# Kernel tuning notes

Hardware: AMD Instinct MI355X
Metric: run time of the kernel (lower is better)

Reference implementation:

```python
import jax, jax.numpy as jnp
import numpy as np

B, C, L, V, H, HEADS, ITERS = 8, 2048, 3, 512, 256, 8, 8
HD = H // HEADS
MAX_LIT = 1024  # literal embedding table holds 2*MAX_LIT rows


def _lin(x, W, b):
    return x @ W.T + b


def _gelu(x):
    return jax.nn.gelu(x, approximate=False)  # torch nn.GELU default = exact erf


def _ln(x, g, b):
    m = x.mean(-1, keepdims=True)
    v = ((x - m) ** 2).mean(-1, keepdims=True)
    return (x - m) / jnp.sqrt(v + 1e-5) * g + b


def setup_inputs() -> dict:
    key = jax.random.key(0)
    ks = jax.random.split(key, 16)
    s = 0.02
    p = {}
    p["formula"] = jax.random.randint(ks[0], (B, C, L), 0, 2 * V)
    p["lit_emb"] = jax.random.normal(ks[1], (2 * MAX_LIT, H)) * s
    # clause_encoder: Linear(H,2H) -> LayerNorm(2H) -> GELU -> Linear(2H,H)
    p["ce_w1"] = jax.random.normal(ks[2], (2 * H, H)) * s
    p["ce_b1"] = jnp.zeros((2 * H,))
    p["ce_g"] = jnp.ones((2 * H,))
    p["ce_beta"] = jnp.zeros((2 * H,))
    p["ce_w2"] = jax.random.normal(ks[3], (H, 2 * H)) * s
    p["ce_b2"] = jnp.zeros((H,))
    # clause_var_attention (nn.MultiheadAttention, eval mode -> no dropout)
    p["attn_in_w"] = jax.random.normal(ks[4], (3 * H, H)) * s
    p["attn_in_b"] = jnp.zeros((3 * H,))
    p["attn_out_w"] = jax.random.normal(ks[5], (H, H)) * s
    p["attn_out_b"] = jnp.zeros((H,))
    # variable_selector: Linear -> GELU -> Linear(H,1)
    p["vs_w1"] = jax.random.normal(ks[6], (H, H)) * s
    p["vs_b1"] = jnp.zeros((H,))
    p["vs_w2"] = jax.random.normal(ks[7], (1, H)) * s
    p["vs_b2"] = jnp.zeros((1,))
    # assignment_predictor: Linear -> GELU -> Linear(H,2) -> Softmax
    p["ap_w1"] = jax.random.normal(ks[8], (H, H)) * s
    p["ap_b1"] = jnp.zeros((H,))
    p["ap_w2"] = jax.random.normal(ks[9], (2, H)) * s
    p["ap_b2"] = jnp.zeros((2,))
    # sat_predictor: Linear -> GELU -> Linear(H,1) -> Sigmoid
    p["sp_w1"] = jax.random.normal(ks[10], (H, H)) * s
    p["sp_b1"] = jnp.zeros((H,))
    p["sp_w2"] = jax.random.normal(ks[11], (1, H)) * s
    p["sp_b2"] = jnp.zeros((1,))
    return p


def _mha(q, kv, in_w, in_b, out_w, out_b):
    Wq, Wk, Wv = jnp.split(in_w, 3, axis=0)
    bq, bk, bv = jnp.split(in_b, 3, axis=0)
    Bq, Nq, _ = q.shape
    Nk = kv.shape[1]
    qh = _lin(q, Wq, bq).reshape(Bq, Nq, HEADS, HD).transpose(0, 2, 1, 3)
    kh = _lin(kv, Wk, bk).reshape(Bq, Nk, HEADS, HD).transpose(0, 2, 1, 3)
    vh = _lin(kv, Wv, bv).reshape(Bq, Nk, HEADS, HD).transpose(0, 2, 1, 3)
    attn = jax.nn.softmax(jnp.einsum("bhqd,bhkd->bhqk", qh, kh) / np.float32(np.sqrt(HD)), axis=-1)
    o = jnp.einsum("bhqk,bhkd->bhqd", attn, vh).transpose(0, 2, 1, 3).reshape(Bq, Nq, H)
    return _lin(o, out_w, out_b)


def reference(formula, lit_emb, ce_w1, ce_b1, ce_g, ce_beta, ce_w2, ce_b2,
              attn_in_w, attn_in_b, attn_out_w, attn_out_b,
              vs_w1, vs_b1, vs_w2, vs_b2, ap_w1, ap_b1, ap_w2, ap_b2,
              sp_w1, sp_b1, sp_w2, sp_b2):
    bidx = jnp.arange(B)
    lit_e = lit_emb[formula]  # [B,C,L,H]
    # clause_encoder output is assignment-independent -> hoist out of the loop
    base = _lin(_gelu(_ln(_lin(lit_e.mean(2), ce_w1, ce_b1), ce_g, ce_beta)), ce_w2, ce_b2)  # [B,C,H]
    var_idx = formula // 2  # [B,C,L]
    pol = formula % 2

    def step(carry, _):
        assignments, var_states, done = carry
        va = assignments[bidx[:, None, None], var_idx]          # [B,C,L] gather
        sat = jnp.any((va == pol) & (va != 2), -1)              # [B,C]
        clause_states = base * (1.0 - 0.9 * sat[..., None].astype(base.dtype))
        vs = _mha(var_states, clause_states, attn_in_w, attn_in_b, attn_out_w, attn_out_b)  # [B,V,H]
        scores = _lin(_gelu(_lin(vs, vs_w1, vs_b1)), vs_w2, vs_b2)[..., 0]  # [B,V]
        scores = scores + (assignments != 2).astype(scores.dtype) * (-1e9)
        sel = jnp.argmax(scores, 1)                             # [B]
        sel_states = vs[bidx, sel]
        probs = jax.nn.softmax(_lin(_gelu(_lin(sel_states, ap_w1, ap_b1)), ap_w2, ap_b2), -1)
        new_a = jnp.argmax(probs, 1).astype(assignments.dtype)
        a2 = assignments.at[bidx, sel].set(new_a)
        # conflict check with updated assignments
        va2 = a2[bidx[:, None, None], var_idx]
        sat2 = jnp.any((va2 == pol) & (va2 != 2), -1)
        conflicting = jnp.all(va2 != 2, -1) & ~sat2             # [B,C]
        any_conf = jnp.any(conflicting)                         # global, as in torch list check
        a3 = jnp.where(any_conf, a2.at[bidx, sel].set(2), a2)   # unassign selected var on conflict
        finished = jnp.all(a3 != 2) & ~any_conf                 # torch early-break condition
        assignments_n = jnp.where(done, assignments, a3)        # freeze after break
        vs_n = jnp.where(done, var_states, vs)
        return (assignments_n, vs_n, done | finished), None

    init = (jnp.full((B, V), 2, jnp.int32), jnp.zeros((B, V, H), base.dtype), jnp.array(False))
    (assignments, var_states, _), _ = jax.lax.scan(step, init, None, length=ITERS)
    is_sat = jax.nn.sigmoid(_lin(_gelu(_lin(var_states.mean(1), sp_w1, sp_b1)), sp_w2, sp_b2))  # [B,1]
    return is_sat, assignments
```

## Files before the change

kernel.cpp:

```cpp
#include <hip/hip_runtime.h>
#include <hip/hip_bf16.h>

#pragma clang fp contract(off)

#define DEVI __device__ __forceinline__

constexpr int Bc = 8, Cc = 2048, Vc = 512, Hc = 256;

constexpr int W_N = 23;
constexpr int W_OFF[W_N] = {
  0,        524288,  655360,  655872,  656384,  656896,  787968,  788224,
  984832,   985600,  1051136, 1051392, 1116928, 1117184, 1117440, 1117444,
  1182980,  1183236, 1183748, 1183752, 1249288, 1249544, 1249800 };
constexpr int W_SZ[W_N] = {
  524288, 131072, 512, 512, 512, 131072, 256, 196608, 768,
  65536, 256, 65536, 256, 256, 1, 65536, 256, 512, 2, 65536, 256, 256, 1 };
constexpr int W_TOT = 1249804;

constexpr size_t WT1_O   = 1249808;
constexpr size_t WT2_O   = WT1_O   + 131072;
constexpr size_t WTIN_O  = WT2_O   + 131072;
constexpr size_t WTOUT_O = WTIN_O  + 196608;
constexpr size_t WTV1_O  = WTOUT_O + 65536;
constexpr size_t WTAP_O  = WTV1_O  + 65536;
constexpr size_t WTSP_O  = WTAP_O  + 65536;
constexpr size_t WCK_O   = WTSP_O  + 65536;
constexpr size_t WCV_O   = WCK_O   + 131072;
constexpr size_t BCK_O   = WCV_O   + 131072;
constexpr size_t BCV_O   = BCK_O   + 256;
constexpr size_t KB_O    = BCV_O   + 256;
constexpr size_t VB_O    = KB_O    + 4194304;
constexpr size_t OO8_O   = VB_O    + 4194304;
constexpr size_t VS8_O   = OO8_O   + 2048;
constexpr size_t FTOT    = VS8_O   + 2048;

constexpr int T_N = 7;
constexpr int T_SRC[T_N]  = { 524288, 656896, 788224, 985600, 1051392, 1117444, 1183752 };
constexpr size_t T_DST[T_N] = { WT1_O, WT2_O, WTIN_O, WTOUT_O, WTV1_O, WTAP_O, WTSP_O };
constexpr int T_ROWS[T_N] = { 512, 256, 768, 256, 256, 256, 256 };
constexpr int T_L2C[T_N]  = { 8, 9, 8, 8, 8, 8, 8 };
constexpr int T_CUM[T_N + 1] = { 0, 131072, 262144, 458752, 524288, 589824, 655360, 720896 };

struct SrcPtrs { const void* p[W_N]; };

DEVI float gelu_ref(float x) {
  return (x * (erff(x / 1.41421356237309504880f) + 1.0f)) * 0.5f;
}

__global__ __launch_bounds__(256) void k_detect(const unsigned short* __restrict__ lit,
                                                int* __restrict__ dflag) {
  __shared__ int red[256];
  int t = threadIdx.x, c = 0;
  for (int i = t; i < 4096; i += 256) {
    unsigned e = (lit[i] >> 7) & 0xFF;
    if (e >= 0x8F) c++;
  }
  red[t] = c;
  __syncthreads();
  for (int s = 128; s > 0; s >>= 1) {
    if (t < s) red[t] += red[t + s];
    __syncthreads();
  }
  if (t == 0) dflag[0] = (red[0] > 64) ? 1 : 0;
}

__global__ __launch_bounds__(256) void k_convert(SrcPtrs sp, float* __restrict__ wf,
                                                 const int* __restrict__ dflag) {
  int idx = blockIdx.x * 256 + threadIdx.x;
  if (idx >= W_TOT) return;
  const int isf32 = dflag[0];
  int i = 0;
  while (i + 1 < W_N && idx >= W_OFF[i + 1]) i++;
  int j = idx - W_OFF[i];
  float v = 0.f;
  if (j < W_SZ[i]) {
    if (isf32) v = ((const float*)sp.p[i])[j];
    else {
      unsigned int u = (unsigned int)((const unsigned short*)sp.p[i])[j] << 16;
      v = __uint_as_float(u);
    }
  }
  wf[idx] = v;
}

__global__ __launch_bounds__(256) void k_transpose(float* __restrict__ wf) {
  int idx = blockIdx.x * 256 + threadIdx.x;
  if (idx >= T_CUM[T_N]) return;
  int mi = 0;
  while (mi + 1 < T_N && idx >= T_CUM[mi + 1]) mi++;
  int local = idx - T_CUM[mi];
  int cols = 1 << T_L2C[mi];
  int r = local >> T_L2C[mi];
  int c = local & (cols - 1);
  wf[T_DST[mi] + (size_t)c * T_ROWS[mi] + r] = wf[T_SRC[mi] + (size_t)local];
}

__global__ __launch_bounds__(256) void k_combine(float* __restrict__ wf) {
  const int blk = blockIdx.x, t = threadIdx.x;
  const float* wtin = wf + WTIN_O;
  if (blk < 512) {
    __shared__ float w2row[256];
    w2row[t] = wf[WT2_O + (size_t)blk * 256 + t];
    __syncthreads();
    float aK = 0.f, aV = 0.f;
    for (int m = 0; m < 256; ++m) {
      float w2 = w2row[m];
      aK = fmaf(w2, wtin[(size_t)m * 768 + 256 + t], aK);
      aV = fmaf(w2, wtin[(size_t)m * 768 + 512 + t], aV);
    }
    wf[WCK_O + (size_t)blk * 256 + t] = aK;
    wf[WCV_O + (size_t)blk * 256 + t] = aV;
  } else {
    float aK = 0.f, aV = 0.f;
    for (int m = 0; m < 256; ++m) {
      float b2 = wf[W_OFF[6] + m];
      aK = fmaf(b2, wtin[(size_t)m * 768 + 256 + t], aK);
      aV = fmaf(b2, wtin[(size_t)m * 768 + 512 + t], aV);
    }
    wf[BCK_O + t] = aK;
    wf[BCV_O + t] = aV;
  }
}

__global__ __launch_bounds__(256) void k_init(float* __restrict__ vs8,
    int* __restrict__ assign, int* __restrict__ flags) {
  int idx = blockIdx.x * 256 + threadIdx.x;
  assign[idx] = 2;
  if (idx < 2048) vs8[idx] = 0.f;
  if (idx < 3) flags[idx] = 0;
}

__global__ __launch_bounds__(256) void k_base(const int* __restrict__ formula,
    const float* __restrict__ wf, float* __restrict__ Kb, float* __restrict__ Vb) {
  __shared__ __align__(16) float xs[16][256];
  __shared__ __align__(16) float h1[16][516];
  __shared__ float mv[16], vr[16];
  const int t = threadIdx.x;
  const int n0 = blockIdx.x * 16;
  const float* lit = wf + W_OFF[0];
  for (int r = 0; r < 16; ++r) {
    int n = n0 + r;
    int f0 = formula[n*3+0], f1 = formula[n*3+1], f2 = formula[n*3+2];
    xs[r][t] = (lit[f0*256 + t] + lit[f1*256 + t] + lit[f2*256 + t]) / 3.0f;
  }
  __syncthreads();
  {
    const float* w1t = wf + WT1_O;
    float a0[16], a1[16];
    #pragma unroll
    for (int r = 0; r < 16; ++r) { a0[r] = 0.f; a1[r] = 0.f; }
    for (int k = 0; k < 256; k += 4) {
      float wa0 = w1t[(size_t)(k+0)*512 + t], wa1 = w1t[(size_t)(k+1)*512 + t];
      float wa2 = w1t[(size_t)(k+2)*512 + t], wa3 = w1t[(size_t)(k+3)*512 + t];
      float wb0 = w1t[(size_t)(k+0)*512 + 256 + t], wb1 = w1t[(size_t)(k+1)*512 + 256 + t];
      float wb2 = w1t[(size_t)(k+2)*512 + 256 + t], wb3 = w1t[(size_t)(k+3)*512 + 256 + t];
      #pragma unroll
      for (int r = 0; r < 16; ++r) {
        float4 x4 = *(const float4*)&xs[r][k];
        a0[r] = fmaf(x4.x, wa0, a0[r]);
        a0[r] = fmaf(x4.y, wa1, a0[r]);
        a0[r] = fmaf(x4.z, wa2, a0[r]);
        a0[r] = fmaf(x4.w, wa3, a0[r]);
        a1[r] = fmaf(x4.x, wb0, a1[r]);
        a1[r] = fmaf(x4.y, wb1, a1[r]);
        a1[r] = fmaf(x4.z, wb2, a1[r]);
        a1[r] = fmaf(x4.w, wb3, a1[r]);
      }
    }
    float b0 = wf[W_OFF[2] + t], b1b = wf[W_OFF[2] + t + 256];
    #pragma unroll
    for (int r = 0; r < 16; ++r) {
      h1[r][t] = a0[r] + b0;
      h1[r][t + 256] = a1[r] + b1b;
    }
  }
  __syncthreads();
  if (t < 16) {
    float s = 0.f;
    for (int k = 0; k < 512; ++k) s += h1[t][k];
    float m = s / 512.0f;
    float v = 0.f;
    for (int k = 0; k < 512; ++k) { float d = h1[t][k] - m; float d2 = d * d; v += d2; }
    mv[t] = m; vr[t] = v / 512.0f;
  }
  __syncthreads();
  {
    const float* g  = wf + W_OFF[3];
    const float* be = wf + W_OFF[4];
    for (int r = 0; r < 16; ++r) {
      float sd = sqrtf(vr[r] + 1e-5f);
      for (int c = t; c < 512; c += 256) {
        float val = (h1[r][c] - mv[r]) / sd * g[c] + be[c];
        h1[r][c] = gelu_ref(val);
      }
    }
  }
  __syncthreads();
  {
    const float* wck = wf + WCK_O;
    const float* wcv = wf + WCV_O;
    float aK[16], aV[16];
    #pragma unroll
    for (int r = 0; r < 16; ++r) { aK[r] = 0.f; aV[r] = 0.f; }
    for (int k = 0; k < 512; k += 4) {
      float ck0 = wck[(size_t)(k+0)*256 + t], ck1 = wck[(size_t)(k+1)*256 + t];
      float ck2 = wck[(size_t)(k+2)*256 + t], ck3 = wck[(size_t)(k+3)*256 + t];
      float cv0 = wcv[(size_t)(k+0)*256 + t], cv1 = wcv[(size_t)(k+1)*256 + t];
      float cv2 = wcv[(size_t)(k+2)*256 + t], cv3 = wcv[(size_t)(k+3)*256 + t];
      #pragma unroll
      for (int r = 0; r < 16; ++r) {
        float4 x4 = *(const float4*)&h1[r][k];
        aK[r] = fmaf(x4.x, ck0, aK[r]);
        aK[r] = fmaf(x4.y, ck1, aK[r]);
        aK[r] = fmaf(x4.z, ck2, aK[r]);
        aK[r] = fmaf(x4.w, ck3, aK[r]);
        aV[r] = fmaf(x4.x, cv0, aV[r]);
        aV[r] = fmaf(x4.y, cv1, aV[r]);
        aV[r] = fmaf(x4.z, cv2, aV[r]);
        aV[r] = fmaf(x4.w, cv3, aV[r]);
      }
    }
    float bck = wf[BCK_O + t], bcv = wf[BCV_O + t];
    const int h = t >> 5, d = t & 31;
    for (int r = 0; r < 16; ++r) {
      int n = n0 + r;
      int b = n >> 11, j = n & 2047;
      size_t off = ((size_t)(b * 8 + h) * 2048 + j) * 32 + d;
      Kb[off] = aK[r] + bck;
      Vb[off] = aV[r] + bcv;
    }
  }
}

__global__ __launch_bounds__(256) void k_attn8(const int* __restrict__ formula,
    const int* __restrict__ assign, const float* __restrict__ Kb,
    const float* __restrict__ Vb, const float* __restrict__ wf,
    const float* __restrict__ vs8, float* __restrict__ oo8,
    const int* __restrict__ flags) {
  if (flags[0]) return;
  __shared__ float xv[256], qs[32];
  __shared__ float sS[2048];
  __shared__ float sF[2048];
  __shared__ float sRed[256];
  __shared__ float sO[8][32];
  __shared__ float sM, sL, sQB;
  const int bh = blockIdx.x, b = bh >> 3, h = bh & 7;
  const int t = threadIdx.x;
  const float FAC1 = 1.0f - 0.9f;

  xv[t] = vs8[b * 256 + t];
  __syncthreads();
  if (t < 32) {
    const float* wt = wf + WTIN_O;
    const int c = h * 32 + t;
    float acc = 0.f;
    for (int k = 0; k < 256; ++k) acc = fmaf(xv[k], wt[(size_t)k * 768 + c], acc);
    qs[t] = acc + wf[W_OFF[8] + c];
  }
  __syncthreads();
  if (t == 0) {
    const float* bk = wf + W_OFF[8] + 256;
    float s = 0.f;
    for (int d = 0; d < 32; ++d) s = fmaf(qs[d], bk[h * 32 + d], s);
    sQB = s;
  }
  __syncthreads();
  float qreg[32];
  #pragma unroll
  for (int d = 0; d < 32; ++d) qreg[d] = qs[d];
  const float qb = sQB;
  const float* kbh = Kb + (size_t)bh * 2048 * 32;
  const float* vbh = Vb + (size_t)bh * 2048 * 32;

  float mloc = -3.402823466e38f;
  for (int i = 0; i < 8; ++i) {
    int j = i * 256 + t;
    int n = b * 2048 + j;
    bool sat = false;
    #pragma unroll
    for (int l = 0; l < 3; ++l) {
      int f = formula[n * 3 + l];
      int a = assign[b * 512 + (f >> 1)];
      sat = sat || (a == (f & 1));
    }
    float fac = sat ? FAC1 : 1.0f;
    const float4* kr4 = (const float4*)(kbh + (size_t)j * 32);
    float p = 0.f;
    #pragma unroll
    for (int g = 0; g < 8; ++g) {
      float4 kk = kr4[g];
      p = fmaf(qreg[4*g+0], kk.x, p);
      p = fmaf(qreg[4*g+1], kk.y, p);
      p = fmaf(qreg[4*g+2], kk.z, p);
      p = fmaf(qreg[4*g+3], kk.w, p);
    }
    float s = fmaf(fac, p, qb);
    sS[j] = s; sF[j] = fac;
    mloc = fmaxf(mloc, s);
  }
  sRed[t] = mloc;
  __syncthreads();
  for (int st = 128; st > 0; st >>= 1) {
    if (t < st) sRed[t] = fmaxf(sRed[t], sRed[t + st]);
    __syncthreads();
  }
  if (t == 0) sM = sRed[0];
  __syncthreads();
  const float M = sM;

  float lloc = 0.f;
  for (int i = 0; i < 8; ++i) {
    int j = t * 8 + i;
    float u = expf(sS[j] - M);
    lloc += u;
    sS[j] = u * sF[j];
  }
  __syncthreads();
  sRed[t] = lloc;
  __syncthreads();
  for (int st = 128; st > 0; st >>= 1) {
    if (t < st) sRed[t] = sRed[t] + sRed[t + st];
    __syncthreads();
  }
  if (t == 0) sL = sRed[0];
  __syncthreads();
  const float L = sL;

  {
    const int jg = t >> 5, d = t & 31;
    float acc = 0.f;
    const float* vbase = vbh + (size_t)(jg * 256) * 32 + d;
    for (int jj = 0; jj < 256; ++jj)
      acc = fmaf(sS[jg * 256 + jj], vbase[(size_t)jj * 32], acc);
    sO[jg][d] = acc;
  }
  __syncthreads();
  if (t < 32) {
    float o = sO[0][t];
    #pragma unroll
    for (int g = 1; g < 8; ++g) o += sO[g][t];
    float bv = wf[W_OFF[8] + 512 + h * 32 + t];
    oo8[b * 256 + h * 32 + t] = o / L + bv;
  }
}

__global__ __launch_bounds__(256) void k_update(const int* __restrict__ formula,
    const float* __restrict__ oo8, const float* __restrict__ wf,
    float* __restrict__ vs8, int* __restrict__ assign, int* __restrict__ selb,
    int* __restrict__ flags) {
  if (flags[0]) return;
  const int b = blockIdx.x, t = threadIdx.x;
  __shared__ float xv[256], hh[256];
  __shared__ int ssel, sna;
  if (t == 0) ssel = 512;
  {
    __shared__ float xo[256];
    xo[t] = oo8[b * 256 + t];
    __syncthreads();
    const float* wt = wf + WTOUT_O;
    float acc = 0.f;
    for (int k = 0; k < 256; ++k) acc = fmaf(xo[k], wt[(size_t)k * 256 + t], acc);
    float v = acc + wf[W_OFF[10] + t];
    vs8[b * 256 + t] = v;
    xv[t] = v;
  }
  __syncthreads();
  for (int i = t; i < 512; i += 256)
    if (assign[b * 512 + i] == 2) atomicMin(&ssel, i);
  __syncthreads();
  const int sel = (ssel == 512) ? 0 : ssel;
  {
    const float* wt = wf + WTAP_O;
    float a = 0.f;
    for (int k = 0; k < 256; ++k) a = fmaf(xv[k], wt[(size_t)k * 256 + t], a);
    hh[t] = gelu_ref(a + wf[W_OFF[16] + t]);
  }
  __syncthreads();
  if (t == 0) {
    const float* w2 = wf + W_OFF[17];
    float l0 = 0.f, l1 = 0.f;
    for (int k = 0; k < 256; ++k) l0 = fmaf(hh[k], w2[k], l0);
    for (int k = 0; k < 256; ++k) l1 = fmaf(hh[k], w2[256 + k], l1);
    l0 += wf[W_OFF[18]];
    l1 += wf[W_OFF[18] + 1];
    int na = (l1 > l0) ? 1 : 0;
    assign[b * 512 + sel] = na;
    selb[b] = sel;
    sna = na;
  }
  __syncthreads();
  const int na = sna;
  int conf = 0, una = 0;
  for (int i = t; i < 2048; i += 256) {
    int n = b * 2048 + i;
    bool sat = false, alla = true;
    #pragma unroll
    for (int l = 0; l < 3; ++l) {
      int f = formula[n * 3 + l];
      int v = f >> 1;
      int a = (v == sel) ? na : assign[b * 512 + v];
      sat = sat || (a == (f & 1));
      alla = alla && (a != 2);
    }
    if (alla && !sat) conf = 1;
  }
  for (int i = t; i < 512; i += 256) {
    int a = (i == sel) ? na : assign[b * 512 + i];
    if (a == 2) una = 1;
  }
  if (conf) atomicOr(&flags[1], 1);
  if (una) atomicOr(&flags[2], 1);
}

__global__ __launch_bounds__(64) void k_fin(int* __restrict__ assign,
    const int* __restrict__ selb, int* __restrict__ flags) {
  if (flags[0]) return;
  const int t = threadIdx.x;
  const int ac = flags[1], ua = flags[2];
  __syncthreads();
  if (ac && t < 8) assign[t * 512 + selb[t]] = 2;
  if (t == 0) {
    if (!ac && !ua) flags[0] = 1;
    flags[1] = 0;
    flags[2] = 0;
  }
}

__global__ __launch_bounds__(256) void k_issat(const float* __restrict__ vs8,
    const int* __restrict__ assign, const float* __restrict__ wf,
    void* __restrict__ outv, const int* __restrict__ dflag) {
  const int b = blockIdx.x, t = threadIdx.x;
  const int isf32 = dflag[0];
  __shared__ float x[256], h[256];
  x[t] = vs8[b * 256 + t];
  __syncthreads();
  const float* wt = wf + WTSP_O;
  float a = 0.f;
  for (int k = 0; k < 256; ++k) a = fmaf(x[k], wt[(size_t)k * 256 + t], a);
  h[t] = gelu_ref(a + wf[W_OFF[20] + t]);
  __syncthreads();
  if (t == 0) {
    const float* w2 = wf + W_OFF[21];
    float l = 0.f;
    for (int k = 0; k < 256; ++k) l = fmaf(h[k], w2[k], l);
    l += wf[W_OFF[22]];
    float sig = 1.f / (1.f + expf(-l));
    if (isf32) ((float*)outv)[b] = sig;
    else ((__hip_bfloat16*)outv)[b] = __float2bfloat16(sig);
  }
  for (int i = t; i < 512; i += 256) {
    float av = (float)assign[b * 512 + i];
    if (isf32) ((float*)outv)[8 + b * 512 + i] = av;
    else ((__hip_bfloat16*)outv)[8 + b * 512 + i] = __float2bfloat16(av);
  }
}

extern "C" void kernel_launch(void* const* d_in, const int* in_sizes, int n_in,
                              void* d_out, int out_size, void* d_ws, size_t ws_size,
                              hipStream_t stream) {
  (void)in_sizes; (void)n_in; (void)out_size; (void)ws_size;
  const int* formula = (const int*)d_in[0];
  float* wf = (float*)d_ws;
  SrcPtrs sp;
  for (int i = 0; i < W_N; ++i) sp.p[i] = d_in[i + 1];
  float* Kb   = wf + KB_O;
  float* Vb   = wf + VB_O;
  float* oo8  = wf + OO8_O;
  float* vs8  = wf + VS8_O;
  int* iw     = (int*)(wf + FTOT);
  int* assign = iw;
  int* selb   = iw + 4096;
  int* flags  = iw + 4104;
  int* dflag  = iw + 4107;

  k_detect<<<1, 256, 0, stream>>>((const unsigned short*)d_in[1], dflag);
  k_convert<<<(W_TOT + 255) / 256, 256, 0, stream>>>(sp, wf, dflag);
  k_transpose<<<(T_CUM[T_N] + 255) / 256, 256, 0, stream>>>(wf);
  k_combine<<<513, 256, 0, stream>>>(wf);
  k_init<<<16, 256, 0, stream>>>(vs8, assign, flags);
  k_base<<<1024, 256, 0, stream>>>(formula, wf, Kb, Vb);
  for (int it = 0; it < 8; ++it) {
    k_attn8<<<64, 256, 0, stream>>>(formula, assign, Kb, Vb, wf, vs8, oo8, flags);
    k_update<<<8, 256, 0, stream>>>(formula, oo8, wf, vs8, assign, selb, flags);
    k_fin<<<1, 64, 0, stream>>>(assign, selb, flags);
  }
  k_issat<<<8, 256, 0, stream>>>(vs8, assign, wf, d_out, dflag);
}
```

Before: 876.3 us.

## Split attention over key chunks and vectorize weight reads in base encoder

The per-iteration attention kernel now splits each (batch, head) over four key chunks, giving 256 blocks instead of 64. Each block writes a partial output, max and sum, and the update kernel merges them with a log-sum-exp rescale. Separately, the clause encoder matmuls now read weights row-major per thread as float4, using the original W1 and a transposed combined K/V weight, in place of coalesced scalar loads. This raises parallelism in the latency-bound iteration loop at the cost of an extra merge step. The float4 per-thread row reads are strided across threads and may coalesce worse.

```diff
diff --git a/kernel.cpp b/kernel.cpp
--- a/kernel.cpp
+++ b/kernel.cpp
@@ -30,9 +30,11 @@
 constexpr size_t BCV_O   = BCK_O   + 256;
 constexpr size_t KB_O    = BCV_O   + 256;
 constexpr size_t VB_O    = KB_O    + 4194304;
-constexpr size_t OO8_O   = VB_O    + 4194304;
-constexpr size_t VS8_O   = OO8_O   + 2048;
-constexpr size_t FTOT    = VS8_O   + 2048;
+constexpr size_t VS8_O   = VB_O    + 4194304;
+constexpr size_t OP_O    = VS8_O   + 2048;
+constexpr size_t PM_O    = OP_O    + 8192;
+constexpr size_t PL_O    = PM_O    + 256;
+constexpr size_t FTOT    = PL_O    + 256;
 
 constexpr int T_N = 7;
 constexpr int T_SRC[T_N]  = { 524288, 656896, 788224, 985600, 1051392, 1117444, 1183752 };
@@ -108,8 +110,8 @@
       aK = fmaf(w2, wtin[(size_t)m * 768 + 256 + t], aK);
       aV = fmaf(w2, wtin[(size_t)m * 768 + 512 + t], aV);
     }
-    wf[WCK_O + (size_t)blk * 256 + t] = aK;
-    wf[WCV_O + (size_t)blk * 256 + t] = aV;
+    wf[WCK_O + (size_t)t * 512 + blk] = aK;
+    wf[WCV_O + (size_t)t * 512 + blk] = aV;
   } else {
     float aK = 0.f, aV = 0.f;
     for (int m = 0; m < 256; ++m) {
@@ -145,26 +147,24 @@
   }
   __syncthreads();
   {
-    const float* w1t = wf + WT1_O;
+    const float4* wa4p = (const float4*)(wf + W_OFF[1] + (size_t)t * 256);
+    const float4* wb4p = (const float4*)(wf + W_OFF[1] + (size_t)(t + 256) * 256);
     float a0[16], a1[16];
     #pragma unroll
     for (int r = 0; r < 16; ++r) { a0[r] = 0.f; a1[r] = 0.f; }
-    for (int k = 0; k < 256; k += 4) {
-      float wa0 = w1t[(size_t)(k+0)*512 + t], wa1 = w1t[(size_t)(k+1)*512 + t];
-      float wa2 = w1t[(size_t)(k+2)*512 + t], wa3 = w1t[(size_t)(k+3)*512 + t];
-      float wb0 = w1t[(size_t)(k+0)*512 + 256 + t], wb1 = w1t[(size_t)(k+1)*512 + 256 + t];
-      float wb2 = w1t[(size_t)(k+2)*512 + 256 + t], wb3 = w1t[(size_t)(k+3)*512 + 256 + t];
+    for (int k4 = 0; k4 < 64; ++k4) {
+      float4 wa = wa4p[k4], wb = wb4p[k4];
       #pragma unroll
       for (int r = 0; r < 16; ++r) {
-        float4 x4 = *(const float4*)&xs[r][k];
-        a0[r] = fmaf(x4.x, wa0, a0[r]);
-        a0[r] = fmaf(x4.y, wa1, a0[r]);
-        a0[r] = fmaf(x4.z, wa2, a0[r]);
-        a0[r] = fmaf(x4.w, wa3, a0[r]);
-        a1[r] = fmaf(x4.x, wb0, a1[r]);
-        a1[r] = fmaf(x4.y, wb1, a1[r]);
-        a1[r] = fmaf(x4.z, wb2, a1[r]);
-        a1[r] = fmaf(x4.w, wb3, a1[r]);
+        float4 x4 = *(const float4*)&xs[r][k4 * 4];
+        a0[r] = fmaf(x4.x, wa.x, a0[r]);
+        a0[r] = fmaf(x4.y, wa.y, a0[r]);
+        a0[r] = fmaf(x4.z, wa.z, a0[r]);
+        a0[r] = fmaf(x4.w, wa.w, a0[r]);
+        a1[r] = fmaf(x4.x, wb.x, a1[r]);
+        a1[r] = fmaf(x4.y, wb.y, a1[r]);
+        a1[r] = fmaf(x4.z, wb.z, a1[r]);
+        a1[r] = fmaf(x4.w, wb.w, a1[r]);
       }
     }
     float b0 = wf[W_OFF[2] + t], b1b = wf[W_OFF[2] + t + 256];
@@ -197,27 +197,24 @@
   }
   __syncthreads();
   {
-    const float* wck = wf + WCK_O;
-    const float* wcv = wf + WCV_O;
+    const float4* ckp = (const float4*)(wf + WCK_O + (size_t)t * 512);
+    const float4* cvp = (const float4*)(wf + WCV_O + (size_t)t * 512);
     float aK[16], aV[16];
     #pragma unroll
     for (int r = 0; r < 16; ++r) { aK[r] = 0.f; aV[r] = 0.f; }
-    for (int k = 0; k < 512; k += 4) {
-      float ck0 = wck[(size_t)(k+0)*256 + t], ck1 = wck[(size_t)(k+1)*256 + t];
-      float ck2 = wck[(size_t)(k+2)*256 + t], ck3 = wck[(size_t)(k+3)*256 + t];
-      float cv0 = wcv[(size_t)(k+0)*256 + t], cv1 = wcv[(size_t)(k+1)*256 + t];
-      float cv2 = wcv[(size_t)(k+2)*256 + t], cv3 = wcv[(size_t)(k+3)*256 + t];
+    for (int k4 = 0; k4 < 128; ++k4) {
+      float4 ck = ckp[k4], cv = cvp[k4];
       #pragma unroll
       for (int r = 0; r < 16; ++r) {
-        float4 x4 = *(const float4*)&h1[r][k];
-        aK[r] = fmaf(x4.x, ck0, aK[r]);
-        aK[r] = fmaf(x4.y, ck1, aK[r]);
-        aK[r] = fmaf(x4.z, ck2, aK[r]);
-        aK[r] = fmaf(x4.w, ck3, aK[r]);
-        aV[r] = fmaf(x4.x, cv0, aV[r]);
-        aV[r] = fmaf(x4.y, cv1, aV[r]);
-        aV[r] = fmaf(x4.z, cv2, aV[r]);
-        aV[r] = fmaf(x4.w, cv3, aV[r]);
+        float4 x4 = *(const float4*)&h1[r][k4 * 4];
+        aK[r] = fmaf(x4.x, ck.x, aK[r]);
+        aK[r] = fmaf(x4.y, ck.y, aK[r]);
+        aK[r] = fmaf(x4.z, ck.z, aK[r]);
+        aK[r] = fmaf(x4.w, ck.w, aK[r]);
+        aV[r] = fmaf(x4.x, cv.x, aV[r]);
+        aV[r] = fmaf(x4.y, cv.y, aV[r]);
+        aV[r] = fmaf(x4.z, cv.z, aV[r]);
+        aV[r] = fmaf(x4.w, cv.w, aV[r]);
       }
     }
     float bck = wf[BCK_O + t], bcv = wf[BCV_O + t];
@@ -232,19 +229,20 @@
   }
 }
 
-__global__ __launch_bounds__(256) void k_attn8(const int* __restrict__ formula,
+__global__ __launch_bounds__(256) void k_attn_part(const int* __restrict__ formula,
     const int* __restrict__ assign, const float* __restrict__ Kb,
     const float* __restrict__ Vb, const float* __restrict__ wf,
-    const float* __restrict__ vs8, float* __restrict__ oo8,
-    const int* __restrict__ flags) {
+    const float* __restrict__ vs8, float* __restrict__ op, float* __restrict__ pm,
+    float* __restrict__ pl, const int* __restrict__ flags) {
   if (flags[0]) return;
   __shared__ float xv[256], qs[32];
-  __shared__ float sS[2048];
-  __shared__ float sF[2048];
+  __shared__ float sS[512], sF[512];
   __shared__ float sRed[256];
   __shared__ float sO[8][32];
-  __shared__ float sM, sL, sQB;
-  const int bh = blockIdx.x, b = bh >> 3, h = bh & 7;
+  __shared__ float sM, sQB;
+  const int blk = blockIdx.x;
+  const int bh = blk >> 2, c = blk & 3;
+  const int b = bh >> 3, h = bh & 7;
   const int t = threadIdx.x;
   const float FAC1 = 1.0f - 0.9f;
 
@@ -252,10 +250,10 @@
   __syncthreads();
   if (t < 32) {
     const float* wt = wf + WTIN_O;
-    const int c = h * 32 + t;
+    const int cc = h * 32 + t;
     float acc = 0.f;
-    for (int k = 0; k < 256; ++k) acc = fmaf(xv[k], wt[(size_t)k * 768 + c], acc);
-    qs[t] = acc + wf[W_OFF[8] + c];
+    for (int k = 0; k < 256; ++k) acc = fmaf(xv[k], wt[(size_t)k * 768 + cc], acc);
+    qs[t] = acc + wf[W_OFF[8] + cc];
   }
   __syncthreads();
   if (t == 0) {
@@ -273,8 +271,10 @@
   const float* vbh = Vb + (size_t)bh * 2048 * 32;
 
   float mloc = -3.402823466e38f;
-  for (int i = 0; i < 8; ++i) {
-    int j = i * 256 + t;
+  #pragma unroll
+  for (int i = 0; i < 2; ++i) {
+    int jl = i * 256 + t;
+    int j = c * 512 + jl;
     int n = b * 2048 + j;
     bool sat = false;
     #pragma unroll
@@ -295,7 +295,7 @@
       p = fmaf(qreg[4*g+3], kk.w, p);
     }
     float s = fmaf(fac, p, qb);
-    sS[j] = s; sF[j] = fac;
+    sS[jl] = s; sF[jl] = fac;
     mloc = fmaxf(mloc, s);
   }
   sRed[t] = mloc;
@@ -306,32 +306,28 @@
   }
   if (t == 0) sM = sRed[0];
   __syncthreads();
-  const float M = sM;
-
-  float lloc = 0.f;
-  for (int i = 0; i < 8; ++i) {
-    int j = t * 8 + i;
-    float u = expf(sS[j] - M);
-    lloc += u;
-    sS[j] = u * sF[j];
-  }
-  __syncthreads();
-  sRed[t] = lloc;
-  __syncthreads();
-  for (int st = 128; st > 0; st >>= 1) {
-    if (t < st) sRed[t] = sRed[t] + sRed[t + st];
+  const float Mc = sM;
+
+  {
+    float u0 = expf(sS[t * 2] - Mc);
+    float u1 = expf(sS[t * 2 + 1] - Mc);
+    float ll = u0 + u1;
+    sS[t * 2] = u0 * sF[t * 2];
+    sS[t * 2 + 1] = u1 * sF[t * 2 + 1];
     __syncthreads();
-  }
-  if (t == 0) sL = sRed[0];
-  __syncthreads();
-  const float L = sL;
-
+    sRed[t] = ll;
+    __syncthreads();
+    for (int st = 128; st > 0; st >>= 1) {
+      if (t < st) sRed[t] = sRed[t] + sRed[t + st];
+      __syncthreads();
+    }
+  }
   {
     const int jg = t >> 5, d = t & 31;
     float acc = 0.f;
-    const float* vbase = vbh + (size_t)(jg * 256) * 32 + d;
-    for (int jj = 0; jj < 256; ++jj)
-      acc = fmaf(sS[jg * 256 + jj], vbase[(size_t)jj * 32], acc);
+    const float* vbase = vbh + (size_t)(c * 512 + jg * 64) * 32 + d;
+    for (int jj = 0; jj < 64; ++jj)
+      acc = fmaf(sS[jg * 64 + jj], vbase[(size_t)jj * 32], acc);
     sO[jg][d] = acc;
   }
   __syncthreads();
@@ -339,24 +335,39 @@
     float o = sO[0][t];
     #pragma unroll
     for (int g = 1; g < 8; ++g) o += sO[g][t];
-    float bv = wf[W_OFF[8] + 512 + h * 32 + t];
-    oo8[b * 256 + h * 32 + t] = o / L + bv;
+    op[(size_t)(bh * 4 + c) * 32 + t] = o;
+    if (t == 0) { pm[bh * 4 + c] = Mc; pl[bh * 4 + c] = sRed[0]; }
   }
 }
 
 __global__ __launch_bounds__(256) void k_update(const int* __restrict__ formula,
-    const float* __restrict__ oo8, const float* __restrict__ wf,
+    const float* __restrict__ op, const float* __restrict__ pm,
+    const float* __restrict__ pl, const float* __restrict__ wf,
     float* __restrict__ vs8, int* __restrict__ assign, int* __restrict__ selb,
     int* __restrict__ flags) {
   if (flags[0]) return;
   const int b = blockIdx.x, t = threadIdx.x;
-  __shared__ float xv[256], hh[256];
+  __shared__ float xo[256], xv[256], hh[256];
   __shared__ int ssel, sna;
   if (t == 0) ssel = 512;
   {
-    __shared__ float xo[256];
-    xo[t] = oo8[b * 256 + t];
-    __syncthreads();
+    const int h = t >> 5, d = t & 31, bh = b * 8 + h;
+    float m0 = pm[bh*4+0], m1 = pm[bh*4+1], m2 = pm[bh*4+2], m3 = pm[bh*4+3];
+    float M = fmaxf(fmaxf(m0, m1), fmaxf(m2, m3));
+    float e0 = expf(m0 - M), e1 = expf(m1 - M), e2 = expf(m2 - M), e3 = expf(m3 - M);
+    float den = e0 * pl[bh*4+0];
+    den = fmaf(e1, pl[bh*4+1], den);
+    den = fmaf(e2, pl[bh*4+2], den);
+    den = fmaf(e3, pl[bh*4+3], den);
+    float O = e0 * op[(size_t)(bh*4+0)*32 + d];
+    O = fmaf(e1, op[(size_t)(bh*4+1)*32 + d], O);
+    O = fmaf(e2, op[(size_t)(bh*4+2)*32 + d], O);
+    O = fmaf(e3, op[(size_t)(bh*4+3)*32 + d], O);
+    float bv = wf[W_OFF[8] + 512 + h * 32 + d];
+    xo[h * 32 + d] = O / den + bv;
+  }
+  __syncthreads();
+  {
     const float* wt = wf + WTOUT_O;
     float acc = 0.f;
     for (int k = 0; k < 256; ++k) acc = fmaf(xo[k], wt[(size_t)k * 256 + t], acc);
@@ -465,8 +476,10 @@
   for (int i = 0; i < W_N; ++i) sp.p[i] = d_in[i + 1];
   float* Kb   = wf + KB_O;
   float* Vb   = wf + VB_O;
-  float* oo8  = wf + OO8_O;
   float* vs8  = wf + VS8_O;
+  float* op   = wf + OP_O;
+  float* pm   = wf + PM_O;
+  float* pl   = wf + PL_O;
   int* iw     = (int*)(wf + FTOT);
   int* assign = iw;
   int* selb   = iw + 4096;
@@ -480,8 +493,8 @@
   k_init<<<16, 256, 0, stream>>>(vs8, assign, flags);
   k_base<<<1024, 256, 0, stream>>>(formula, wf, Kb, Vb);
   for (int it = 0; it < 8; ++it) {
-    k_attn8<<<64, 256, 0, stream>>>(formula, assign, Kb, Vb, wf, vs8, oo8, flags);
-    k_update<<<8, 256, 0, stream>>>(formula, oo8, wf, vs8, assign, selb, flags);
+    k_attn_part<<<256, 256, 0, stream>>>(formula, assign, Kb, Vb, wf, vs8, op, pm, pl, flags);
+    k_update<<<8, 256, 0, stream>>>(formula, op, pm, pl, wf, vs8, assign, selb, flags);
     k_fin<<<1, 64, 0, stream>>>(assign, selb, flags);
   }
   k_issat<<<8, 256, 0, stream>>>(vs8, assign, wf, d_out, dflag);
```

Result: slower. 965.4 us (+10.2%).
